# Optimization experiments

Hardware: AMD Instinct MI355X
Metric: run time of the kernel (lower is better)

## Reference

```python
import jax, jax.numpy as jnp
import numpy as np

B, N, D, E, G, MID, OUT = 8, 256, 128, 128, 128, 128, 128


def setup_inputs() -> dict:
    key = jax.random.key(0)
    ks = jax.random.split(key, 20)
    s = 0.02
    inp = {
        'node_fts': jax.random.normal(ks[0], (B, N, D), jnp.float32),
        'edge_fts': jax.random.normal(ks[1], (B, N, N, E), jnp.float32),
        'graph_fts': jax.random.normal(ks[2], (B, G), jnp.float32),
        'adj_mat': jax.random.randint(ks[3], (B, N, N), 0, 2, jnp.int32),
        'hidden': jax.random.normal(ks[4], (B, N, D), jnp.float32),
        # message linears (m_n_1, m_h_1, m_e_1, m_g_1)
        'Wn': s * jax.random.normal(ks[5], (D, MID), jnp.float32),
        'bn': jnp.zeros((MID,), jnp.float32),
        'Wh': s * jax.random.normal(ks[6], (D, MID), jnp.float32),
        'bh': jnp.zeros((MID,), jnp.float32),
        'We': s * jax.random.normal(ks[7], (E, MID), jnp.float32),
        'be': jnp.zeros((MID,), jnp.float32),
        'Wg': s * jax.random.normal(ks[8], (G, MID), jnp.float32),
        'bg': jnp.zeros((MID,), jnp.float32),
        # output linears o1 (node), o2 (hidden), o3 (msgs)
        'Wo1': s * jax.random.normal(ks[9], (D, OUT), jnp.float32),
        'bo1': jnp.zeros((OUT,), jnp.float32),
        'Wo2': s * jax.random.normal(ks[10], (D, OUT), jnp.float32),
        'bo2': jnp.zeros((OUT,), jnp.float32),
        'Wo3': s * jax.random.normal(ks[11], (MID, OUT), jnp.float32),
        'bo3': jnp.zeros((OUT,), jnp.float32),
    }
    return inp


def reference(node_fts, edge_fts, graph_fts, adj_mat, hidden,
              Wn, bn, Wh, bh, We, be, Wg, bg,
              Wo1, bo1, Wo2, bo2, Wo3, bo3):
    # Linear projections feeding the broadcast message tensor
    msg_n = node_fts @ Wn + bn          # (B, N, MID)
    msg_h = hidden @ Wh + bh            # (B, N, MID)
    msg_e = edge_fts @ We + be          # (B, N, N, MID)
    msg_g = graph_fts @ Wg + bg         # (B, MID)

    # Broadcast-add into (B, N, N, MID): axis1 <- msg_n (sender), axis2 <- msg_h
    msgs = (msg_n[:, None, :, :] + msg_h[:, :, None, :]
            + msg_e + msg_g[:, None, None, :])

    # Masked max-reduce over axis 1 (msgs_mlp_sizes is None -> no MLP)
    adj = adj_mat.astype(msgs.dtype)[..., None]  # (B, N, N, 1)
    msgs = jnp.max(msgs * adj, axis=1)           # (B, N, MID)

    ret = (node_fts @ Wo1 + bo1) + (hidden @ Wo2 + bo2) + (msgs @ Wo3 + bo3)
    return ret
```

## Files before the change

kernel.cpp:

```cpp
#include <hip/hip_runtime.h>
#include <hip/hip_bf16.h>

#define B_ 8
#define N_ 256
#define C_ 128
#define S_ 8
#define STEPB (N_ * C_ * 4)

typedef __attribute__((ext_vector_type(4))) float f32x4;
typedef __attribute__((ext_vector_type(8))) short s16x8;

typedef __attribute__((address_space(1))) const void gas_void;
typedef __attribute__((address_space(3))) void las_void;

__device__ __forceinline__ unsigned short f2bf(float f) {
  unsigned int u = __builtin_bit_cast(unsigned int, f);
  u += 0x7FFFu + ((u >> 16) & 1u);
  return (unsigned short)(u >> 16);
}

__device__ __forceinline__ unsigned int pk2(float a, float b) {
  __hip_bfloat162 h = __float22bfloat162_rn(make_float2(a, b));
  unsigned int u;
  __builtin_memcpy(&u, &h, 4);
  return u;
}

__device__ __forceinline__ s16x8 cvt8(f32x4 lo, f32x4 hi) {
  union { unsigned int u[4]; s16x8 s; } r;
  r.u[0] = pk2(lo[0], lo[1]);
  r.u[1] = pk2(lo[2], lo[3]);
  r.u[2] = pk2(hi[0], hi[1]);
  r.u[3] = pk2(hi[2], hi[3]);
  return r.s;
}

__global__ void k_pro(const float* __restrict__ node, const float* __restrict__ hidden,
                      const float* __restrict__ graph, const int* __restrict__ adjm,
                      const float* __restrict__ Wn, const float* __restrict__ bn,
                      const float* __restrict__ Wh, const float* __restrict__ bh,
                      const float* __restrict__ be,
                      const float* __restrict__ Wg, const float* __restrict__ bg,
                      const float* __restrict__ We,
                      float* __restrict__ ws_c, unsigned short* __restrict__ ws_mh2,
                      short* __restrict__ ws_B, unsigned char* __restrict__ ws_adj) {
  int bid = blockIdx.x, t = threadIdx.x;
  if (bid >= 544) {
    int base = (bid - 544) * 1024 + t * 8;
    int4 a = *reinterpret_cast<const int4*>(adjm + base);
    int4 c = *reinterpret_cast<const int4*>(adjm + base + 4);
    uint2 v;
    v.x = (unsigned)a.x | ((unsigned)a.y << 8) | ((unsigned)a.z << 16) | ((unsigned)a.w << 24);
    v.y = (unsigned)c.x | ((unsigned)c.y << 8) | ((unsigned)c.z << 16) | ((unsigned)c.w << 24);
    *reinterpret_cast<uint2*>(ws_adj + base) = v;
    return;
  }
  if (bid >= 512) {
    int f = bid - 512;
    if (t < 64) {
      int kb = f >> 3, nbg = f & 7;
      int lr = t & 15, lg = t >> 4;
      s16x8 v;
#pragma unroll
      for (int e = 0; e < 8; ++e)
        v[e] = (short)f2bf(We[(kb * 32 + lg * 8 + e) * C_ + nbg * 16 + lr]);
      *reinterpret_cast<s16x8*>(ws_B + (f * 64 + t) * 8) = v;
    }
    return;
  }
  bool isc = bid < 256;
  int row0 = (isc ? bid : bid - 256) * 8;
  const float* src = isc ? node : hidden;
  const float* W   = isc ? Wn : Wh;
  __shared__ float sh[8][C_];
#pragma unroll
  for (int r = 0; r < 8; ++r) sh[r][t] = src[(row0 + r) * C_ + t];
  __syncthreads();
  float g = 0.f;
  float acc[8];
#pragma unroll
  for (int r = 0; r < 8; ++r) acc[r] = 0.f;
  const float* gr = graph + (row0 >> 8) * C_;
  for (int k = 0; k < C_; k += 8) {
    float wv[8];
#pragma unroll
    for (int u = 0; u < 8; ++u) wv[u] = W[(k + u) * C_ + t];
    if (isc) {
      float wgv[8];
#pragma unroll
      for (int u = 0; u < 8; ++u) wgv[u] = Wg[(k + u) * C_ + t];
#pragma unroll
      for (int u = 0; u < 8; ++u) g += gr[k + u] * wgv[u];
    }
#pragma unroll
    for (int u = 0; u < 8; ++u)
#pragma unroll
      for (int r = 0; r < 8; ++r) acc[r] += sh[r][k + u] * wv[u];
  }
  if (isc) {
    float init = bn[t] + be[t] + bg[t] + g;
#pragma unroll
    for (int r = 0; r < 8; ++r) ws_c[(row0 + r) * C_ + t] = acc[r] + init;
  } else {
    float init = bh[t];
    int p = (t >> 5) * 32 + (t & 15) * 2 + ((t >> 4) & 1);
#pragma unroll
    for (int r = 0; r < 8; ++r) ws_mh2[(row0 + r) * C_ + p] = f2bf(acc[r] + init);
  }
}

__global__ __launch_bounds__(256, 4) void k_main(
    const float* __restrict__ edge, const unsigned char* __restrict__ ws_adj,
    const short* __restrict__ ws_B,
    const float* __restrict__ ws_c, const unsigned short* __restrict__ ws_mh2,
    float* __restrict__ pbuf) {
  __shared__ __align__(16) char smem[3 * 8192 + 8192 + 512];
  char* ring    = smem;
  char* mh_lds  = smem + 24576;
  char* adj_lds = smem + 24576 + 8192;
  const int lane = threadIdx.x & 63;
  const int w = threadIdx.x >> 6;
  const int wg = blockIdx.x;
  const int b   = wg & 7;
  const int j16 = (wg >> 3) & 15;
  const int s   = wg >> 7;
  const int j0 = j16 * 16;
  const int n0 = w * 32;
  const int lr = lane & 15;
  const int lg = lane >> 4;

  s16x8 bfrag[4][2];
#pragma unroll
  for (int kb = 0; kb < 4; ++kb)
#pragma unroll
    for (int nb = 0; nb < 2; ++nb)
      bfrag[kb][nb] = *reinterpret_cast<const s16x8*>(
          ws_B + ((kb * 8 + w * 2 + nb) * 64 + lane) * 8);

  float cf[2][4];
#pragma unroll
  for (int nb = 0; nb < 2; ++nb)
#pragma unroll
    for (int r = 0; r < 4; ++r)
      cf[nb][r] = ws_c[(b * N_ + j0 + lg * 4 + r) * C_ + n0 + nb * 16 + lr];

  f32x4 mx[2];
#pragma unroll
  for (int nb = 0; nb < 2; ++nb)
#pragma unroll
    for (int r = 0; r < 4; ++r) mx[nb][r] = -INFINITY;

  const char* gedge = (const char*)(edge + ((size_t)(b * N_ + s) * N_ + j0) * C_);

  int soff[2];
#pragma unroll
  for (int q = 0; q < 2; ++q) {
    int y = w * 2048 + q * 1024 + lane * 16;
    int row = y >> 9;
    soff[q] = y ^ ((row & 7) << 4);
  }
  const int base0 = lr * 512 + lg * 32;
  const int swz = (lr & 7) << 4;

#define GLL16(GP, LP) __builtin_amdgcn_global_load_lds((gas_void*)(GP), (las_void*)(LP), 16, 0, 0)
#define GLL4(GP, LP)  __builtin_amdgcn_global_load_lds((gas_void*)(GP), (las_void*)(LP), 4, 0, 0)

#define ISSUE(SL, TT) do { \
    const char* gch = gedge + (size_t)(TT) * 8 * STEPB; \
    char* lb = ring + (SL) * 8192 + w * 2048; \
    GLL16(gch + soff[0], lb); \
    GLL16(gch + soff[1], lb + 1024); \
  } while (0)

#define STEP(SL, ISL, WAITN, DOISSUE, TI, T) do { \
    asm volatile("s_waitcnt vmcnt(" WAITN ")\n\ts_barrier" ::: "memory"); \
    if (DOISSUE) ISSUE(ISL, TI); \
    const char* rb = ring + (SL) * 8192; \
    s16x8 af[4]; \
    _Pragma("unroll") \
    for (int kb = 0; kb < 4; ++kb) { \
      int a0 = (base0 + kb * 128) ^ swz; \
      f32x4 lo = *reinterpret_cast<const f32x4*>(rb + a0); \
      f32x4 hi = *reinterpret_cast<const f32x4*>(rb + (a0 ^ 16)); \
      af[kb] = cvt8(lo, hi); \
    } \
    unsigned int mw = *reinterpret_cast<const unsigned int*>(mh_lds + (T) * 256 + w * 64 + lr * 4); \
    unsigned int ab = *reinterpret_cast<const unsigned int*>(adj_lds + (T) * 16 + lg * 4); \
    float mh0 = __builtin_bit_cast(float, mw << 16); \
    float mh1 = __builtin_bit_cast(float, mw & 0xffff0000u); \
    float adjf[4] = {(float)(ab & 0xff), (float)((ab >> 8) & 0xff), \
                     (float)((ab >> 16) & 0xff), (float)(ab >> 24)}; \
    _Pragma("unroll") \
    for (int nb = 0; nb < 2; ++nb) { \
      f32x4 acc; \
      float mhv = nb ? mh1 : mh0; \
      _Pragma("unroll") \
      for (int r = 0; r < 4; ++r) acc[r] = cf[nb][r] + mhv; \
      _Pragma("unroll") \
      for (int kb = 0; kb < 4; ++kb) \
        acc = __builtin_amdgcn_mfma_f32_16x16x32_bf16(af[kb], bfrag[kb][nb], acc, 0, 0, 0); \
      _Pragma("unroll") \
      for (int r = 0; r < 4; ++r) mx[nb][r] = fmaxf(mx[nb][r], adjf[r] * acc[r]); \
    } \
  } while (0)

  {
    const char* mh_g = (const char*)(ws_mh2 + (size_t)b * N_ * C_);
#pragma unroll
    for (int q = 0; q < 2; ++q) {
      int T = w * 8 + q * 4 + (lane >> 4);
      GLL16(mh_g + ((size_t)(s + 8 * T)) * 256 + (lane & 15) * 16,
            mh_lds + w * 2048 + q * 1024);
    }
    const char* adj_g = (const char*)(ws_adj + (size_t)b * N_ * N_ + j0);
    GLL4(adj_g + ((size_t)(s + 8 * (lane >> 2))) * N_ + (lane & 3) * 4, adj_lds);
    GLL4(adj_g + ((size_t)(s + 8 * (16 + (lane >> 2)))) * N_ + (lane & 3) * 4, adj_lds + 256);
  }
  ISSUE(0, 0);
  ISSUE(1, 1);
  asm volatile("s_waitcnt vmcnt(4)\n\ts_barrier" ::: "memory");

  for (int o = 0; o < 10; ++o) {
    STEP(0, 2, "2", 1, 3 * o + 2, 3 * o);
    STEP(1, 0, "2", 1, 3 * o + 3, 3 * o + 1);
    STEP(2, 1, "2", 1, 3 * o + 4, 3 * o + 2);
  }
  STEP(0, 2, "2", 0, 0, 30);
  STEP(1, 0, "0", 0, 0, 31);

#undef STEP
#undef ISSUE
#undef GLL16
#undef GLL4

  float* prow = pbuf + (((size_t)s * B_ + b) * N_ + j0 + lg * 4) * C_ + n0 + lr;
#pragma unroll
  for (int nb = 0; nb < 2; ++nb)
#pragma unroll
    for (int r = 0; r < 4; ++r)
      prow[r * C_ + nb * 16] = mx[nb][r];
}

__global__ void k_epi(const float* __restrict__ node, const float* __restrict__ hidden,
                      const float* __restrict__ Wo1, const float* __restrict__ bo1,
                      const float* __restrict__ Wo2, const float* __restrict__ bo2,
                      const float* __restrict__ Wo3, const float* __restrict__ bo3,
                      const float* __restrict__ pbuf, float* __restrict__ out) {
  int row0 = blockIdx.x * 4;
  int col = threadIdx.x & 127;
  int half = threadIdx.x >> 7;
  __shared__ float shn[4][C_], shh[4][C_], shm[4][C_];
#pragma unroll
  for (int r = 0; r < 2; ++r) {
    int rr = half * 2 + r;
    shn[rr][col] = node[(row0 + rr) * C_ + col];
    shh[rr][col] = hidden[(row0 + rr) * C_ + col];
    float mv = -INFINITY;
#pragma unroll
    for (int s = 0; s < S_; ++s)
      mv = fmaxf(mv, pbuf[((size_t)s * (B_ * N_) + row0 + rr) * C_ + col]);
    shm[rr][col] = mv;
  }
  __syncthreads();
  float init = bo1[col] + bo2[col] + bo3[col];
  float acc[2];
  acc[0] = init; acc[1] = init;
  for (int k = 0; k < C_; k += 8) {
    float wv1[8], wv2[8], wv3[8];
#pragma unroll
    for (int u = 0; u < 8; ++u) {
      wv1[u] = Wo1[(k + u) * C_ + col];
      wv2[u] = Wo2[(k + u) * C_ + col];
      wv3[u] = Wo3[(k + u) * C_ + col];
    }
#pragma unroll
    for (int u = 0; u < 8; ++u)
#pragma unroll
      for (int r = 0; r < 2; ++r) {
        int rr = half * 2 + r;
        acc[r] += shn[rr][k + u] * wv1[u] + shh[rr][k + u] * wv2[u] + shm[rr][k + u] * wv3[u];
      }
  }
#pragma unroll
  for (int r = 0; r < 2; ++r)
    out[(row0 + half * 2 + r) * C_ + col] = acc[r];
}

extern "C" void kernel_launch(void* const* d_in, const int* in_sizes, int n_in,
                              void* d_out, int out_size, void* d_ws, size_t ws_size,
                              hipStream_t stream) {
  const float* node   = (const float*)d_in[0];
  const float* edge   = (const float*)d_in[1];
  const float* graph  = (const float*)d_in[2];
  const int*   adjm   = (const int*)d_in[3];
  const float* hidden = (const float*)d_in[4];
  const float* Wn = (const float*)d_in[5];  const float* bn = (const float*)d_in[6];
  const float* Wh = (const float*)d_in[7];  const float* bh = (const float*)d_in[8];
  const float* We = (const float*)d_in[9];  const float* be = (const float*)d_in[10];
  const float* Wg = (const float*)d_in[11]; const float* bg = (const float*)d_in[12];
  const float* Wo1 = (const float*)d_in[13]; const float* bo1 = (const float*)d_in[14];
  const float* Wo2 = (const float*)d_in[15]; const float* bo2 = (const float*)d_in[16];
  const float* Wo3 = (const float*)d_in[17]; const float* bo3 = (const float*)d_in[18];
  float* out = (float*)d_out;

  char* ws = (char*)d_ws;
  float*          ws_c   = (float*)ws;
  unsigned short* ws_mh2 = (unsigned short*)(ws + (1u << 20));
  short*          ws_B   = (short*)(ws + 1572864u);
  unsigned char*  ws_adj = (unsigned char*)(ws + 1835008u);
  float*          pbuf   = (float*)(ws + (4u << 20));

  k_pro<<<1056, 128, 0, stream>>>(node, hidden, graph, adjm, Wn, bn, Wh, bh, be,
                                  Wg, bg, We, ws_c, ws_mh2, ws_B, ws_adj);
  k_main<<<1024, 256, 0, stream>>>(edge, ws_adj, ws_B, ws_c, ws_mh2, pbuf);
  k_epi<<<512, 256, 0, stream>>>(node, hidden, Wo1, bo1, Wo2, bo2, Wo3, bo3,
                                 pbuf, out);
}
```

Baseline: 86.49 us.

## Process 32 receiver columns per block with 512 threads in k_main

```diff
diff --git a/kernel.cpp b/kernel.cpp
--- a/kernel.cpp
+++ b/kernel.cpp
@@ -109,23 +109,25 @@
   }
 }
 
-__global__ __launch_bounds__(256, 4) void k_main(
+__global__ __launch_bounds__(512, 4) void k_main(
     const float* __restrict__ edge, const unsigned char* __restrict__ ws_adj,
     const short* __restrict__ ws_B,
     const float* __restrict__ ws_c, const unsigned short* __restrict__ ws_mh2,
     float* __restrict__ pbuf) {
-  __shared__ __align__(16) char smem[3 * 8192 + 8192 + 512];
+  __shared__ __align__(16) char smem[3 * 16384 + 8192 + 1024];
   char* ring    = smem;
-  char* mh_lds  = smem + 24576;
-  char* adj_lds = smem + 24576 + 8192;
+  char* mh_lds  = smem + 49152;
+  char* adj_lds = smem + 49152 + 8192;
   const int lane = threadIdx.x & 63;
-  const int w = threadIdx.x >> 6;
+  const int w  = threadIdx.x >> 6;
+  const int wq = w & 3;
+  const int jh = w >> 2;
   const int wg = blockIdx.x;
   const int b   = wg & 7;
-  const int j16 = (wg >> 3) & 15;
-  const int s   = wg >> 7;
-  const int j0 = j16 * 16;
-  const int n0 = w * 32;
+  const int j32 = (wg >> 3) & 7;
+  const int s   = wg >> 6;
+  const int j0 = j32 * 32;
+  const int n0 = wq * 32;
   const int lr = lane & 15;
   const int lg = lane >> 4;
 
@@ -135,14 +137,14 @@
 #pragma unroll
     for (int nb = 0; nb < 2; ++nb)
       bfrag[kb][nb] = *reinterpret_cast<const s16x8*>(
-          ws_B + ((kb * 8 + w * 2 + nb) * 64 + lane) * 8);
+          ws_B + ((kb * 8 + wq * 2 + nb) * 64 + lane) * 8);
 
   float cf[2][4];
 #pragma unroll
   for (int nb = 0; nb < 2; ++nb)
 #pragma unroll
     for (int r = 0; r < 4; ++r)
-      cf[nb][r] = ws_c[(b * N_ + j0 + lg * 4 + r) * C_ + n0 + nb * 16 + lr];
+      cf[nb][r] = ws_c[(b * N_ + j0 + jh * 16 + lg * 4 + r) * C_ + n0 + nb * 16 + lr];
 
   f32x4 mx[2];
 #pragma unroll
@@ -159,15 +161,14 @@
     int row = y >> 9;
     soff[q] = y ^ ((row & 7) << 4);
   }
-  const int base0 = lr * 512 + lg * 32;
+  const int base0 = (jh * 16 + lr) * 512 + lg * 32;
   const int swz = (lr & 7) << 4;
 
 #define GLL16(GP, LP) __builtin_amdgcn_global_load_lds((gas_void*)(GP), (las_void*)(LP), 16, 0, 0)
-#define GLL4(GP, LP)  __builtin_amdgcn_global_load_lds((gas_void*)(GP), (las_void*)(LP), 4, 0, 0)
 
 #define ISSUE(SL, TT) do { \
     const char* gch = gedge + (size_t)(TT) * 8 * STEPB; \
-    char* lb = ring + (SL) * 8192 + w * 2048; \
+    char* lb = ring + (SL) * 16384 + w * 2048; \
     GLL16(gch + soff[0], lb); \
     GLL16(gch + soff[1], lb + 1024); \
   } while (0)
@@ -175,7 +176,7 @@
 #define STEP(SL, ISL, WAITN, DOISSUE, TI, T) do { \
     asm volatile("s_waitcnt vmcnt(" WAITN ")\n\ts_barrier" ::: "memory"); \
     if (DOISSUE) ISSUE(ISL, TI); \
-    const char* rb = ring + (SL) * 8192; \
+    const char* rb = ring + (SL) * 16384; \
     s16x8 af[4]; \
     _Pragma("unroll") \
     for (int kb = 0; kb < 4; ++kb) { \
@@ -184,8 +185,8 @@
       f32x4 hi = *reinterpret_cast<const f32x4*>(rb + (a0 ^ 16)); \
       af[kb] = cvt8(lo, hi); \
     } \
-    unsigned int mw = *reinterpret_cast<const unsigned int*>(mh_lds + (T) * 256 + w * 64 + lr * 4); \
-    unsigned int ab = *reinterpret_cast<const unsigned int*>(adj_lds + (T) * 16 + lg * 4); \
+    unsigned int mw = *reinterpret_cast<const unsigned int*>(mh_lds + (T) * 256 + wq * 64 + lr * 4); \
+    unsigned int ab = *reinterpret_cast<const unsigned int*>(adj_lds + (T) * 32 + jh * 16 + lg * 4); \
     float mh0 = __builtin_bit_cast(float, mw << 16); \
     float mh1 = __builtin_bit_cast(float, mw & 0xffff0000u); \
     float adjf[4] = {(float)(ab & 0xff), (float)((ab >> 8) & 0xff), \
@@ -206,15 +207,10 @@
 
   {
     const char* mh_g = (const char*)(ws_mh2 + (size_t)b * N_ * C_);
-#pragma unroll
-    for (int q = 0; q < 2; ++q) {
-      int T = w * 8 + q * 4 + (lane >> 4);
-      GLL16(mh_g + ((size_t)(s + 8 * T)) * 256 + (lane & 15) * 16,
-            mh_lds + w * 2048 + q * 1024);
-    }
+    int T = w * 4 + (lane >> 4);
+    GLL16(mh_g + ((size_t)(s + 8 * T)) * 256 + (lane & 15) * 16, mh_lds + w * 1024);
     const char* adj_g = (const char*)(ws_adj + (size_t)b * N_ * N_ + j0);
-    GLL4(adj_g + ((size_t)(s + 8 * (lane >> 2))) * N_ + (lane & 3) * 4, adj_lds);
-    GLL4(adj_g + ((size_t)(s + 8 * (16 + (lane >> 2)))) * N_ + (lane & 3) * 4, adj_lds + 256);
+    GLL16(adj_g + ((size_t)(s + 8 * (lane >> 1))) * N_ + (lane & 1) * 16, adj_lds);
   }
   ISSUE(0, 0);
   ISSUE(1, 1);
@@ -231,9 +227,8 @@
 #undef STEP
 #undef ISSUE
 #undef GLL16
-#undef GLL4
-
-  float* prow = pbuf + (((size_t)s * B_ + b) * N_ + j0 + lg * 4) * C_ + n0 + lr;
+
+  float* prow = pbuf + (((size_t)s * B_ + b) * N_ + j0 + jh * 16 + lg * 4) * C_ + n0 + lr;
 #pragma unroll
   for (int nb = 0; nb < 2; ++nb)
 #pragma unroll
@@ -312,7 +307,7 @@
 
   k_pro<<<1056, 128, 0, stream>>>(node, hidden, graph, adjm, Wn, bn, Wh, bh, be,
                                   Wg, bg, We, ws_c, ws_mh2, ws_B, ws_adj);
-  k_main<<<1024, 256, 0, stream>>>(edge, ws_adj, ws_B, ws_c, ws_mh2, pbuf);
+  k_main<<<512, 512, 0, stream>>>(edge, ws_adj, ws_B, ws_c, ws_mh2, pbuf);
   k_epi<<<512, 256, 0, stream>>>(node, hidden, Wo1, bo1, Wo2, bo2, Wo3, bo3,
                                  pbuf, out);
 }
```

Result: no change. 85.45 us (-1.2%).

## Skip edge-feature loads for rows whose adjacency entry is zero

Applied to the files above, without the earlier changes.

```diff
diff --git a/kernel.cpp b/kernel.cpp
--- a/kernel.cpp
+++ b/kernel.cpp
@@ -161,6 +161,8 @@
   }
   const int base0 = lr * 512 + lg * 32;
   const int swz = (lr & 7) << 4;
+  const int jrow0 = w * 4 + (lane >> 5);
+  const int jrow1 = jrow0 + 2;
 
 #define GLL16(GP, LP) __builtin_amdgcn_global_load_lds((gas_void*)(GP), (las_void*)(LP), 16, 0, 0)
 #define GLL4(GP, LP)  __builtin_amdgcn_global_load_lds((gas_void*)(GP), (las_void*)(LP), 4, 0, 0)
@@ -172,9 +174,25 @@
     GLL16(gch + soff[1], lb + 1024); \
   } while (0)
 
-#define STEP(SL, ISL, WAITN, DOISSUE, TI, T) do { \
-    asm volatile("s_waitcnt vmcnt(" WAITN ")\n\ts_barrier" ::: "memory"); \
-    if (DOISSUE) ISSUE(ISL, TI); \
+  int cprev = 2;
+
+#define STEPD(SL, ISL, TI, T, DOISSUE) do { \
+    if (cprev == 2)      asm volatile("s_waitcnt vmcnt(2)\n\ts_barrier" ::: "memory"); \
+    else if (cprev == 1) asm volatile("s_waitcnt vmcnt(1)\n\ts_barrier" ::: "memory"); \
+    else                 asm volatile("s_waitcnt vmcnt(0)\n\ts_barrier" ::: "memory"); \
+    if (DOISSUE) { \
+      const char* gch = gedge + (size_t)(TI) * 8 * STEPB; \
+      char* lb = ring + (ISL) * 8192 + w * 2048; \
+      unsigned char av0 = *(const unsigned char*)(adj_lds + (TI) * 16 + jrow0); \
+      unsigned char av1 = *(const unsigned char*)(adj_lds + (TI) * 16 + jrow1); \
+      int u0 = __any((int)av0); \
+      int u1 = __any((int)av1); \
+      if (u0) { if (av0) GLL16(gch + soff[0], lb); } \
+      if (u1) { if (av1) GLL16(gch + soff[1], lb + 1024); } \
+      cprev = u0 + u1; \
+    } else { \
+      cprev = 0; \
+    } \
     const char* rb = ring + (SL) * 8192; \
     s16x8 af[4]; \
     _Pragma("unroll") \
@@ -205,6 +223,10 @@
   } while (0)
 
   {
+    char* z = ring + 2 * 8192 + w * 2048 + lane * 16;
+    f32x4 zero = {0.f, 0.f, 0.f, 0.f};
+    *reinterpret_cast<f32x4*>(z) = zero;
+    *reinterpret_cast<f32x4*>(z + 1024) = zero;
     const char* mh_g = (const char*)(ws_mh2 + (size_t)b * N_ * C_);
 #pragma unroll
     for (int q = 0; q < 2; ++q) {
@@ -218,17 +240,17 @@
   }
   ISSUE(0, 0);
   ISSUE(1, 1);
-  asm volatile("s_waitcnt vmcnt(4)\n\ts_barrier" ::: "memory");
+  asm volatile("s_waitcnt vmcnt(4) lgkmcnt(0)\n\ts_barrier" ::: "memory");
 
   for (int o = 0; o < 10; ++o) {
-    STEP(0, 2, "2", 1, 3 * o + 2, 3 * o);
-    STEP(1, 0, "2", 1, 3 * o + 3, 3 * o + 1);
-    STEP(2, 1, "2", 1, 3 * o + 4, 3 * o + 2);
-  }
-  STEP(0, 2, "2", 0, 0, 30);
-  STEP(1, 0, "0", 0, 0, 31);
-
-#undef STEP
+    STEPD(0, 2, 3 * o + 2, 3 * o,     1);
+    STEPD(1, 0, 3 * o + 3, 3 * o + 1, 1);
+    STEPD(2, 1, 3 * o + 4, 3 * o + 2, 1);
+  }
+  STEPD(0, 2, 0, 30, 0);
+  STEPD(1, 0, 0, 31, 0);
+
+#undef STEPD
 #undef ISSUE
 #undef GLL16
 #undef GLL4
```

After: 80.46 us. -7.0%, faster.
